# Performance work log

Measured on AMD Instinct MI355X. Metric: run time of the kernel, lower is better.

The kernel has to match this reference:

```python
import jax, jax.numpy as jnp
import numpy as np

HIDDEN = 1152
NUM_HEADS = 16
HEAD_DIM = HIDDEN // NUM_HEADS  # 72
BATCH, SEQ = 8, 1024


def setup_inputs() -> dict:
    key = jax.random.key(0)
    ks = jax.random.split(key, 9)
    s = 0.02
    return {
        "x": jax.random.normal(ks[0], (BATCH, SEQ, HIDDEN), dtype=jnp.float32),
        "wq": jax.random.normal(ks[1], (HIDDEN, HIDDEN), dtype=jnp.float32) * s,
        "bq": jax.random.normal(ks[2], (HIDDEN,), dtype=jnp.float32) * s,
        "wk": jax.random.normal(ks[3], (HIDDEN, HIDDEN), dtype=jnp.float32) * s,
        "bk": jax.random.normal(ks[4], (HIDDEN,), dtype=jnp.float32) * s,
        "wv": jax.random.normal(ks[5], (HIDDEN, HIDDEN), dtype=jnp.float32) * s,
        "bv": jax.random.normal(ks[6], (HIDDEN,), dtype=jnp.float32) * s,
        "wo": jax.random.normal(ks[7], (HIDDEN, HIDDEN), dtype=jnp.float32) * s,
        "bo": jax.random.normal(ks[8], (HIDDEN,), dtype=jnp.float32) * s,
    }


def reference(x, wq, bq, wk, bk, wv, bv, wo, bo):
    B, S, H = x.shape
    nh, hd = NUM_HEADS, HEAD_DIM
    # projections (weights stored [in, out] to match nn.Linear x @ W^T with W^T precomposed)
    q = (x @ wq + bq).reshape(B, S, nh, hd).transpose(0, 2, 1, 3)  # [B,nh,S,hd]
    k = (x @ wk + bk).reshape(B, S, nh, hd).transpose(0, 2, 1, 3)
    v = (x @ wv + bv).reshape(B, S, nh, hd).transpose(0, 2, 1, 3)
    scale = 1.0 / jnp.sqrt(jnp.asarray(hd, dtype=x.dtype))
    scores = jnp.einsum("bhqd,bhkd->bhqk", q, k) * scale  # [B,nh,S,S]
    attn = jax.nn.softmax(scores, axis=-1)
    out = jnp.einsum("bhqk,bhkd->bhqd", attn, v)  # [B,nh,S,hd]
    out = out.transpose(0, 2, 1, 3).reshape(B, S, H)
    return out @ wo + bo
```

## Files before the change

### kernel.cpp

```cpp
#include <hip/hip_runtime.h>
#include <hip/hip_bf16.h>

#define HIDDEN 1152
#define NUM_HEADS 16
#define BATCH 8
#define SEQ 1024
#define MROWS (BATCH * SEQ)
#define KSTRIDE 104

typedef __attribute__((ext_vector_type(8))) short short8;
typedef __attribute__((ext_vector_type(4))) float f32x4;

__device__ inline short f2bf(float x) {
  unsigned u = __float_as_uint(x);
  unsigned r = (u + 0x7FFFu + ((u >> 16) & 1u)) >> 16;
  return (short)(r & 0xFFFFu);
}

__device__ inline void gload16(const void* g, void* l) {
  __builtin_amdgcn_global_load_lds(
      (const __attribute__((address_space(1))) void*)g,
      (__attribute__((address_space(3))) void*)l, 16, 0, 0);
}

__global__ __launch_bounds__(256) void k_cvtx(const float* __restrict__ X,
                                              short* __restrict__ Xb) {
  const size_t base = ((size_t)blockIdx.x * 256 + threadIdx.x) * 8;
  float4 a = *(const float4*)(X + base);
  float4 b = *(const float4*)(X + base + 4);
  short8 o = {f2bf(a.x), f2bf(a.y), f2bf(a.z), f2bf(a.w),
              f2bf(b.x), f2bf(b.y), f2bf(b.z), f2bf(b.w)};
  *(short8*)(Xb + base) = o;
}

__global__ __launch_bounds__(256) void k_cvtw(const float* __restrict__ W0,
                                              const float* __restrict__ W1,
                                              const float* __restrict__ W2,
                                              const float* __restrict__ W3,
                                              short* __restrict__ Wt) {
  __shared__ float T[64][65];
  const float* W = (blockIdx.z == 0) ? W0 : (blockIdx.z == 1) ? W1
                 : (blockIdx.z == 2) ? W2 : W3;
  short* dst = Wt + (size_t)blockIdx.z * HIDDEN * HIDDEN;
  const int n0 = blockIdx.x * 64, k0 = blockIdx.y * 64;
  const int tid = threadIdx.x;
  for (int t = tid; t < 4096; t += 256) {
    int r = t >> 6, c = t & 63;
    T[r][c] = W[(size_t)(k0 + r) * HIDDEN + n0 + c];
  }
  __syncthreads();
  for (int t = tid; t < 4096; t += 256) {
    int r = t >> 6, c = t & 63;
    dst[(size_t)(n0 + r) * HIDDEN + k0 + c] = f2bf(T[c][r]);
  }
}

__global__ __launch_bounds__(256) void k_kpad(short* __restrict__ Kp) {
  const int r = blockIdx.x * 256 + threadIdx.x;
  const short8 z = {0, 0, 0, 0, 0, 0, 0, 0};
  short* p = Kp + (size_t)r * KSTRIDE + 72;
  *(short8*)(p) = z;
  *(short8*)(p + 8) = z;
  *(short8*)(p + 16) = z;
}

template <int OUTKIND, int RSTRIDE>
__global__ __launch_bounds__(256) void k_gemm(const short* __restrict__ A,
                                              const short* __restrict__ Bt,
                                              const float* __restrict__ bias,
                                              void* __restrict__ Cout,
                                              float scale) {
  __shared__ __align__(16) short As[8192];
  __shared__ __align__(16) short Bs[8192];
  const int tid = threadIdx.x;
  const int lane = tid & 63;
  const int wid = tid >> 6;
  const int wr = wid >> 1, wc = wid & 1;
  const int flat = blockIdx.y * 9 + blockIdx.x;
  const int rid = (flat & 7) * 72 + (flat >> 3);
  const int row0 = (rid / 9) << 7;
  const int col0 = (rid % 9) << 7;
  const int l15 = lane & 15, lh = lane >> 4;
  const int lr8 = lane >> 3;
  const int csrc = ((lane & 7) ^ lr8) << 3;

  const f32x4 fz = {0.f, 0.f, 0.f, 0.f};
  f32x4 acc[4][4];
#pragma unroll
  for (int m = 0; m < 4; ++m)
#pragma unroll
    for (int n = 0; n < 4; ++n) acc[m][n] = fz;

  for (int k0 = 0; k0 < HIDDEN; k0 += 64) {
#pragma unroll
    for (int i = 0; i < 4; ++i) {
      const int chunk = (wid << 2) + i;
      const int r = (chunk << 3) + lr8;
      gload16(A + (size_t)(row0 + r) * HIDDEN + k0 + csrc, (void*)(As + (chunk << 9)));
      gload16(Bt + (size_t)(col0 + r) * HIDDEN + k0 + csrc, (void*)(Bs + (chunk << 9)));
    }
    __syncthreads();
#pragma unroll
    for (int ks = 0; ks < 2; ++ks) {
      short8 af[4], bfr[4];
#pragma unroll
      for (int m = 0; m < 4; ++m) {
        const int r = (wr << 6) + (m << 4) + l15;
        const int off = ((ks << 6) + (lh << 4)) ^ ((r & 7) << 4);
        af[m] = *(const short8*)((const char*)As + r * 128 + off);
      }
#pragma unroll
      for (int n = 0; n < 4; ++n) {
        const int r = (wc << 6) + (n << 4) + l15;
        const int off = ((ks << 6) + (lh << 4)) ^ ((r & 7) << 4);
        bfr[n] = *(const short8*)((const char*)Bs + r * 128 + off);
      }
      __builtin_amdgcn_s_setprio(1);
#pragma unroll
      for (int m = 0; m < 4; ++m)
#pragma unroll
        for (int n = 0; n < 4; ++n)
          acc[m][n] = __builtin_amdgcn_mfma_f32_16x16x32_bf16(af[m], bfr[n], acc[m][n], 0, 0, 0);
      __builtin_amdgcn_s_setprio(0);
    }
    __syncthreads();
  }

  if (OUTKIND == 0) {
    short* C = (short*)Cout;
#pragma unroll
    for (int n = 0; n < 4; ++n) {
      const int c = col0 + (wc << 6) + (n << 4) + l15;
      const int h = c / 72;
      const int d = c - h * 72;
      const float bv = bias[c];
#pragma unroll
      for (int m = 0; m < 4; ++m)
#pragma unroll
        for (int i = 0; i < 4; ++i) {
          const int r = row0 + (wr << 6) + (m << 4) + (lh << 2) + i;
          const int b = r >> 10, s = r & 1023;
          C[(size_t)((((b << 4) + h) << 10) + s) * RSTRIDE + d] =
              f2bf((acc[m][n][i] + bv) * scale);
        }
    }
  } else {
    float* C = (float*)Cout;
#pragma unroll
    for (int n = 0; n < 4; ++n) {
      const int c = col0 + (wc << 6) + (n << 4) + l15;
      const float bv = bias[c];
#pragma unroll
      for (int m = 0; m < 4; ++m)
#pragma unroll
        for (int i = 0; i < 4; ++i) {
          const int r = row0 + (wr << 6) + (m << 4) + (lh << 2) + i;
          C[(size_t)r * HIDDEN + c] = acc[m][n][i] + bv;
        }
    }
  }
}

__global__ __launch_bounds__(256) void k_vtrans(const short* __restrict__ V,
                                                short* __restrict__ Vt) {
  __shared__ short T[128 * 80];
  const int tid = threadIdx.x;
  const int s0 = blockIdx.x * 128;
  const int bh = blockIdx.y;
  const size_t vbase = (size_t)bh * SEQ * 72;
  for (int t = tid; t < 128 * 9; t += 256) {
    int r = t / 9, ch = t - r * 9;
    *(short8*)(T + r * 80 + ch * 8) =
        *(const short8*)(V + vbase + (size_t)(s0 + r) * 72 + ch * 8);
  }
  __syncthreads();
  const size_t obase = (size_t)bh * 80 * 1024;
  const short8 sz = {0, 0, 0, 0, 0, 0, 0, 0};
  for (int t = tid; t < 80 * 16; t += 256) {
    int sc = t / 80, d = t - sc * 80;
    short8 v = sz;
    if (d < 72) {
#pragma unroll
      for (int j = 0; j < 8; ++j) v[j] = T[(sc * 8 + j) * 80 + d];
    }
    *(short8*)(Vt + obase + (size_t)d * 1024 + s0 + sc * 8) = v;
  }
}

__global__ __launch_bounds__(256, 4) void k_attn(const short* __restrict__ Qg,
                                                 const short* __restrict__ Kp,
                                                 const short* __restrict__ Vt,
                                                 short* __restrict__ Og) {
  __shared__ __align__(16) short Ks[64 * KSTRIDE];
  __shared__ __align__(16) short Vs[80 * 64];
  __shared__ __align__(16) short Ps[4 * 16 * 72];
  const int tid = threadIdx.x, lane = tid & 63, wid = tid >> 6;
  const int l15 = lane & 15, lh = lane >> 4;
  const int id = blockIdx.x;
  const int rid = (id & 7) * 128 + (id >> 3);
  const int bh = rid >> 3;
  const int q0 = (rid & 7) << 7;
  const short8 sz = {0, 0, 0, 0, 0, 0, 0, 0};
  const f32x4 fz = {0.f, 0.f, 0.f, 0.f};

  short8 qf[2][3];
#pragma unroll
  for (int m = 0; m < 2; ++m)
#pragma unroll
    for (int ks = 0; ks < 3; ++ks) {
      const int row = q0 + wid * 32 + m * 16 + l15;
      const int e0 = ks * 32 + lh * 8;
      if (e0 < 72)
        qf[m][ks] = *(const short8*)(Qg + ((size_t)bh * 1024 + row) * 72 + e0);
      else
        qf[m][ks] = sz;
    }

  float mrun[2] = {-1e30f, -1e30f};
  float lrun[2] = {0.f, 0.f};
  f32x4 oacc[2][5];
#pragma unroll
  for (int m = 0; m < 2; ++m)
#pragma unroll
    for (int no = 0; no < 5; ++no) oacc[m][no] = fz;

  const char* kgb = (const char*)Kp + ((size_t)bh * 1024) * (KSTRIDE * 2);
  const char* vgb = (const char*)Vt + (size_t)bh * 163840;

  for (int kt = 0; kt < 16; ++kt) {
    const char* kg = kgb + (size_t)kt * 64 * (KSTRIDE * 2);
    for (int c = wid; c < 13; c += 4)
      gload16(kg + c * 1024 + lane * 16, (char*)Ks + c * 1024);
    for (int c = wid; c < 10; c += 4) {
      const int p = c * 1024 + lane * 16;
      const int d = p >> 7;
      const int sc16 = (lane & 7) ^ (d & 7);
      gload16(vgb + (size_t)d * 2048 + kt * 128 + sc16 * 16, (char*)Vs + c * 1024);
    }
    __syncthreads();

#pragma unroll
    for (int m = 0; m < 2; ++m) {
      f32x4 sa[4];
#pragma unroll
      for (int n = 0; n < 4; ++n) sa[n] = fz;
#pragma unroll
      for (int ks = 0; ks < 3; ++ks) {
        short8 kf[4];
#pragma unroll
        for (int n = 0; n < 4; ++n)
          kf[n] = *(const short8*)((const char*)Ks + (n * 16 + l15) * 208 + ks * 64 + lh * 16);
        __builtin_amdgcn_s_setprio(1);
#pragma unroll
        for (int n = 0; n < 4; ++n)
          sa[n] = __builtin_amdgcn_mfma_f32_16x16x32_bf16(kf[n], qf[m][ks], sa[n], 0, 0, 0);
        __builtin_amdgcn_s_setprio(0);
      }

      float mx = sa[0][0];
#pragma unroll
      for (int n = 0; n < 4; ++n)
#pragma unroll
        for (int i = 0; i < 4; ++i) mx = fmaxf(mx, sa[n][i]);
      mx = fmaxf(mx, __shfl_xor(mx, 16));
      mx = fmaxf(mx, __shfl_xor(mx, 32));

      const bool skip = __all(mx <= mrun[m] + 8.0f);
      if (!skip) {
        const float nm = fmaxf(mrun[m], mx);
        const float corr = __expf(mrun[m] - nm);
        lrun[m] *= corr;
        mrun[m] = nm;
        float c0 = __shfl(corr, lh * 4 + 0);
        float c1 = __shfl(corr, lh * 4 + 1);
        float c2 = __shfl(corr, lh * 4 + 2);
        float c3 = __shfl(corr, lh * 4 + 3);
        const f32x4 cv = {c0, c1, c2, c3};
#pragma unroll
        for (int no = 0; no < 5; ++no) oacc[m][no] *= cv;
      }

      float ps = 0.f;
#pragma unroll
      for (int n = 0; n < 4; ++n)
#pragma unroll
        for (int i = 0; i < 4; ++i) {
          const float p = __expf(sa[n][i] - mrun[m]);
          sa[n][i] = p;
          ps += p;
        }
      ps += __shfl_xor(ps, 16);
      ps += __shfl_xor(ps, 32);
      lrun[m] += ps;

#pragma unroll
      for (int n = 0; n < 4; ++n) {
        unsigned w0 = __builtin_amdgcn_perm(__float_as_uint(sa[n][1]),
                                            __float_as_uint(sa[n][0]), 0x07060302u);
        unsigned w1 = __builtin_amdgcn_perm(__float_as_uint(sa[n][3]),
                                            __float_as_uint(sa[n][2]), 0x07060302u);
        uint2 w = {w0, w1};
        *(uint2*)((char*)Ps + wid * 2304 + l15 * 144 + n * 32 + lh * 8) = w;
      }

#pragma unroll
      for (int ks = 0; ks < 2; ++ks) {
        const short8 pa = *(const short8*)((const char*)Ps + wid * 2304 + l15 * 144 + ks * 64 + lh * 16);
        short8 vb[5];
        const int cc = ((ks << 2) + lh) ^ (l15 & 7);
#pragma unroll
        for (int no = 0; no < 5; ++no)
          vb[no] = *(const short8*)((const char*)Vs + no * 2048 + l15 * 128 + cc * 16);
        __builtin_amdgcn_s_setprio(1);
#pragma unroll
        for (int no = 0; no < 5; ++no)
          oacc[m][no] = __builtin_amdgcn_mfma_f32_16x16x32_bf16(pa, vb[no], oacc[m][no], 0, 0, 0);
        __builtin_amdgcn_s_setprio(0);
      }
    }
    __syncthreads();
  }

  const int b = bh >> 4, h = bh & 15;
#pragma unroll
  for (int m = 0; m < 2; ++m) {
    const float il = 1.0f / lrun[m];
    float inv[4];
#pragma unroll
    for (int i = 0; i < 4; ++i) inv[i] = __shfl(il, lh * 4 + i);
#pragma unroll
    for (int no = 0; no < 5; ++no) {
      const int d = no * 16 + l15;
      if (d < 72) {
#pragma unroll
        for (int i = 0; i < 4; ++i) {
          const int s = q0 + wid * 32 + m * 16 + lh * 4 + i;
          Og[((size_t)(b * 1024 + s)) * HIDDEN + h * 72 + d] = f2bf(oacc[m][no][i] * inv[i]);
        }
      }
    }
  }
}

extern "C" void kernel_launch(void* const* d_in, const int* in_sizes, int n_in,
                              void* d_out, int out_size, void* d_ws, size_t ws_size,
                              hipStream_t stream) {
  const float* x  = (const float*)d_in[0];
  const float* wq = (const float*)d_in[1];
  const float* bq = (const float*)d_in[2];
  const float* wk = (const float*)d_in[3];
  const float* bk = (const float*)d_in[4];
  const float* wv = (const float*)d_in[5];
  const float* bv = (const float*)d_in[6];
  const float* wo = (const float*)d_in[7];
  const float* bo = (const float*)d_in[8];

  char* ws = (char*)d_ws;
  short* xb = (short*)ws;
  short* wT = (short*)(ws + 18874368);
  short* Qb = (short*)(ws + 29491200);
  short* Kp = (short*)(ws + 48365568);
  short* Vb = (short*)(ws + 75628544);
  short* Vt = (short*)(ws + 94502912);
  const size_t WSZ = (size_t)HIDDEN * HIDDEN;

  k_kpad<<<512, 256, 0, stream>>>(Kp);
  k_cvtx<<<4608, 256, 0, stream>>>(x, xb);
  k_cvtw<<<dim3(18, 18, 4), 256, 0, stream>>>(wq, wk, wv, wo, wT);

  dim3 gg(9, 64);
  const float qscale = 0.11785113019775793f;
  k_gemm<0, 72><<<gg, 256, 0, stream>>>(xb, wT + 0 * WSZ, bq, (void*)Qb, qscale);
  k_gemm<0, KSTRIDE><<<gg, 256, 0, stream>>>(xb, wT + 1 * WSZ, bk, (void*)Kp, 1.0f);
  k_gemm<0, 72><<<gg, 256, 0, stream>>>(xb, wT + 2 * WSZ, bv, (void*)Vb, 1.0f);

  k_vtrans<<<dim3(8, 128), 256, 0, stream>>>(Vb, Vt);
  k_attn<<<1024, 256, 0, stream>>>(Qb, Kp, Vt, xb);

  k_gemm<1, 0><<<gg, 256, 0, stream>>>(xb, wT + 3 * WSZ, bo, d_out, 1.0f);
}
```

Measured before the change: 238.3 us.

## Fuse QKV GEMMs, write V transposed directly, drop LDS staging in attention

Merges the three Q/K/V projection GEMMs into one launch over a 27-column-tile grid, with the V tiles writing straight into the transposed, padded layout. This removes the separate V transpose kernel and the K padding kernel. The attention kernel no longer stages K and V tiles through shared memory with barriers and instead reads MFMA fragments directly from global memory, relying on the cache for reuse. That saves LDS traffic and syncs but risks more global and L2 pressure from redundant, less coalesced per-wave loads.

```diff
diff --git a/kernel.cpp b/kernel.cpp
--- a/kernel.cpp
+++ b/kernel.cpp
@@ -6,7 +6,7 @@
 #define BATCH 8
 #define SEQ 1024
 #define MROWS (BATCH * SEQ)
-#define KSTRIDE 104
+#define QSCALE 0.11785113019775793f
 
 typedef __attribute__((ext_vector_type(8))) short short8;
 typedef __attribute__((ext_vector_type(4))) float f32x4;
@@ -55,21 +55,122 @@
   }
 }
 
-__global__ __launch_bounds__(256) void k_kpad(short* __restrict__ Kp) {
-  const int r = blockIdx.x * 256 + threadIdx.x;
+__global__ __launch_bounds__(256) void k_vzero(short* __restrict__ Vt) {
+  const int t = blockIdx.x * 256 + threadIdx.x;
+  const int bh = t >> 10;
+  const int off = (t & 1023) * 8;
   const short8 z = {0, 0, 0, 0, 0, 0, 0, 0};
-  short* p = Kp + (size_t)r * KSTRIDE + 72;
-  *(short8*)(p) = z;
-  *(short8*)(p + 8) = z;
-  *(short8*)(p + 16) = z;
-}
-
-template <int OUTKIND, int RSTRIDE>
-__global__ __launch_bounds__(256) void k_gemm(const short* __restrict__ A,
-                                              const short* __restrict__ Bt,
-                                              const float* __restrict__ bias,
-                                              void* __restrict__ Cout,
-                                              float scale) {
+  *(short8*)(Vt + (size_t)bh * 81920 + 73728 + off) = z;
+}
+
+__global__ __launch_bounds__(256) void k_gemm_qkv(
+    const short* __restrict__ A, const short* __restrict__ Bt,
+    const float* __restrict__ bq, const float* __restrict__ bk,
+    const float* __restrict__ bv, short* __restrict__ Qb,
+    short* __restrict__ Kb, short* __restrict__ Vt) {
+  __shared__ __align__(16) short As[8192];
+  __shared__ __align__(16) short Bs[8192];
+  const int tid = threadIdx.x;
+  const int lane = tid & 63;
+  const int wid = tid >> 6;
+  const int wr = wid >> 1, wc = wid & 1;
+  const int flat = blockIdx.y * 27 + blockIdx.x;
+  const int rid = (flat & 7) * 216 + (flat >> 3);
+  const int row0 = (rid / 27) << 7;
+  const int col0 = (rid % 27) << 7;
+  const int l15 = lane & 15, lh = lane >> 4;
+  const int lr8 = lane >> 3;
+  const int csrc = ((lane & 7) ^ lr8) << 3;
+
+  const f32x4 fz = {0.f, 0.f, 0.f, 0.f};
+  f32x4 acc[4][4];
+#pragma unroll
+  for (int m = 0; m < 4; ++m)
+#pragma unroll
+    for (int n = 0; n < 4; ++n) acc[m][n] = fz;
+
+  for (int k0 = 0; k0 < HIDDEN; k0 += 64) {
+#pragma unroll
+    for (int i = 0; i < 4; ++i) {
+      const int chunk = (wid << 2) + i;
+      const int r = (chunk << 3) + lr8;
+      gload16(A + (size_t)(row0 + r) * HIDDEN + k0 + csrc, (void*)(As + (chunk << 9)));
+      gload16(Bt + (size_t)(col0 + r) * HIDDEN + k0 + csrc, (void*)(Bs + (chunk << 9)));
+    }
+    __syncthreads();
+#pragma unroll
+    for (int ks = 0; ks < 2; ++ks) {
+      short8 af[4], bfr[4];
+#pragma unroll
+      for (int m = 0; m < 4; ++m) {
+        const int r = (wr << 6) + (m << 4) + l15;
+        const int off = ((ks << 6) + (lh << 4)) ^ ((r & 7) << 4);
+        af[m] = *(const short8*)((const char*)As + r * 128 + off);
+      }
+#pragma unroll
+      for (int n = 0; n < 4; ++n) {
+        const int r = (wc << 6) + (n << 4) + l15;
+        const int off = ((ks << 6) + (lh << 4)) ^ ((r & 7) << 4);
+        bfr[n] = *(const short8*)((const char*)Bs + r * 128 + off);
+      }
+      __builtin_amdgcn_s_setprio(1);
+#pragma unroll
+      for (int m = 0; m < 4; ++m)
+#pragma unroll
+        for (int n = 0; n < 4; ++n)
+          acc[m][n] = __builtin_amdgcn_mfma_f32_16x16x32_bf16(af[m], bfr[n], acc[m][n], 0, 0, 0);
+      __builtin_amdgcn_s_setprio(0);
+    }
+    __syncthreads();
+  }
+
+  const int cseg = (rid % 27) / 9;
+  if (cseg < 2) {
+    short* dst = (cseg == 0) ? Qb : Kb;
+    const float* bias = (cseg == 0) ? bq : bk;
+    const float scl = (cseg == 0) ? QSCALE : 1.0f;
+#pragma unroll
+    for (int n = 0; n < 4; ++n) {
+      const int c = col0 - cseg * HIDDEN + (wc << 6) + (n << 4) + l15;
+      const int h = c / 72;
+      const int d = c - h * 72;
+      const float bvx = bias[c];
+#pragma unroll
+      for (int m = 0; m < 4; ++m)
+#pragma unroll
+        for (int i = 0; i < 4; ++i) {
+          const int r = row0 + (wr << 6) + (m << 4) + (lh << 2) + i;
+          const int b = r >> 10, s = r & 1023;
+          dst[(size_t)((((b << 4) + h) << 10) + s) * 72 + d] =
+              f2bf((acc[m][n][i] + bvx) * scl);
+        }
+    }
+  } else {
+#pragma unroll
+    for (int n = 0; n < 4; ++n) {
+      const int c = col0 - 2 * HIDDEN + (wc << 6) + (n << 4) + l15;
+      const int h = c / 72;
+      const int d = c - h * 72;
+      const float bvx = bv[c];
+#pragma unroll
+      for (int m = 0; m < 4; ++m) {
+        const int r0 = row0 + (wr << 6) + (m << 4) + (lh << 2);
+        const int b = r0 >> 10, s0 = r0 & 1023;
+        short4 o;
+        o.x = f2bf(acc[m][n][0] + bvx);
+        o.y = f2bf(acc[m][n][1] + bvx);
+        o.z = f2bf(acc[m][n][2] + bvx);
+        o.w = f2bf(acc[m][n][3] + bvx);
+        *(short4*)(Vt + ((size_t)(((b << 4) + h) * 80 + d) << 10) + s0) = o;
+      }
+    }
+  }
+}
+
+__global__ __launch_bounds__(256) void k_gemm_o(const short* __restrict__ A,
+                                                const short* __restrict__ Bt,
+                                                const float* __restrict__ bias,
+                                                float* __restrict__ C) {
   __shared__ __align__(16) short As[8192];
   __shared__ __align__(16) short Bs[8192];
   const int tid = threadIdx.x;
@@ -126,73 +227,24 @@
     __syncthreads();
   }
 
-  if (OUTKIND == 0) {
-    short* C = (short*)Cout;
-#pragma unroll
-    for (int n = 0; n < 4; ++n) {
-      const int c = col0 + (wc << 6) + (n << 4) + l15;
-      const int h = c / 72;
-      const int d = c - h * 72;
-      const float bv = bias[c];
-#pragma unroll
-      for (int m = 0; m < 4; ++m)
-#pragma unroll
-        for (int i = 0; i < 4; ++i) {
-          const int r = row0 + (wr << 6) + (m << 4) + (lh << 2) + i;
-          const int b = r >> 10, s = r & 1023;
-          C[(size_t)((((b << 4) + h) << 10) + s) * RSTRIDE + d] =
-              f2bf((acc[m][n][i] + bv) * scale);
-        }
-    }
-  } else {
-    float* C = (float*)Cout;
-#pragma unroll
-    for (int n = 0; n < 4; ++n) {
-      const int c = col0 + (wc << 6) + (n << 4) + l15;
-      const float bv = bias[c];
-#pragma unroll
-      for (int m = 0; m < 4; ++m)
-#pragma unroll
-        for (int i = 0; i < 4; ++i) {
-          const int r = row0 + (wr << 6) + (m << 4) + (lh << 2) + i;
-          C[(size_t)r * HIDDEN + c] = acc[m][n][i] + bv;
-        }
-    }
-  }
-}
-
-__global__ __launch_bounds__(256) void k_vtrans(const short* __restrict__ V,
-                                                short* __restrict__ Vt) {
-  __shared__ short T[128 * 80];
-  const int tid = threadIdx.x;
-  const int s0 = blockIdx.x * 128;
-  const int bh = blockIdx.y;
-  const size_t vbase = (size_t)bh * SEQ * 72;
-  for (int t = tid; t < 128 * 9; t += 256) {
-    int r = t / 9, ch = t - r * 9;
-    *(short8*)(T + r * 80 + ch * 8) =
-        *(const short8*)(V + vbase + (size_t)(s0 + r) * 72 + ch * 8);
-  }
-  __syncthreads();
-  const size_t obase = (size_t)bh * 80 * 1024;
-  const short8 sz = {0, 0, 0, 0, 0, 0, 0, 0};
-  for (int t = tid; t < 80 * 16; t += 256) {
-    int sc = t / 80, d = t - sc * 80;
-    short8 v = sz;
-    if (d < 72) {
-#pragma unroll
-      for (int j = 0; j < 8; ++j) v[j] = T[(sc * 8 + j) * 80 + d];
-    }
-    *(short8*)(Vt + obase + (size_t)d * 1024 + s0 + sc * 8) = v;
+#pragma unroll
+  for (int n = 0; n < 4; ++n) {
+    const int c = col0 + (wc << 6) + (n << 4) + l15;
+    const float bvx = bias[c];
+#pragma unroll
+    for (int m = 0; m < 4; ++m)
+#pragma unroll
+      for (int i = 0; i < 4; ++i) {
+        const int r = row0 + (wr << 6) + (m << 4) + (lh << 2) + i;
+        C[(size_t)r * HIDDEN + c] = acc[m][n][i] + bvx;
+      }
   }
 }
 
 __global__ __launch_bounds__(256, 4) void k_attn(const short* __restrict__ Qg,
-                                                 const short* __restrict__ Kp,
+                                                 const short* __restrict__ Kg,
                                                  const short* __restrict__ Vt,
                                                  short* __restrict__ Og) {
-  __shared__ __align__(16) short Ks[64 * KSTRIDE];
-  __shared__ __align__(16) short Vs[80 * 64];
   __shared__ __align__(16) short Ps[4 * 16 * 72];
   const int tid = threadIdx.x, lane = tid & 63, wid = tid >> 6;
   const int l15 = lane & 15, lh = lane >> 4;
@@ -224,21 +276,11 @@
 #pragma unroll
     for (int no = 0; no < 5; ++no) oacc[m][no] = fz;
 
-  const char* kgb = (const char*)Kp + ((size_t)bh * 1024) * (KSTRIDE * 2);
-  const char* vgb = (const char*)Vt + (size_t)bh * 163840;
+  const short* kb = Kg + (size_t)bh * 1024 * 72;
+  const short* vg = Vt + (size_t)bh * 81920;
+  short* psw = Ps + wid * 1152;
 
   for (int kt = 0; kt < 16; ++kt) {
-    const char* kg = kgb + (size_t)kt * 64 * (KSTRIDE * 2);
-    for (int c = wid; c < 13; c += 4)
-      gload16(kg + c * 1024 + lane * 16, (char*)Ks + c * 1024);
-    for (int c = wid; c < 10; c += 4) {
-      const int p = c * 1024 + lane * 16;
-      const int d = p >> 7;
-      const int sc16 = (lane & 7) ^ (d & 7);
-      gload16(vgb + (size_t)d * 2048 + kt * 128 + sc16 * 16, (char*)Vs + c * 1024);
-    }
-    __syncthreads();
-
 #pragma unroll
     for (int m = 0; m < 2; ++m) {
       f32x4 sa[4];
@@ -249,7 +291,8 @@
         short8 kf[4];
 #pragma unroll
         for (int n = 0; n < 4; ++n)
-          kf[n] = *(const short8*)((const char*)Ks + (n * 16 + l15) * 208 + ks * 64 + lh * 16);
+          kf[n] = *(const short8*)(kb + (size_t)(kt * 64 + n * 16 + l15) * 72 +
+                                   ks * 32 + lh * 8);
         __builtin_amdgcn_s_setprio(1);
 #pragma unroll
         for (int n = 0; n < 4; ++n)
@@ -300,17 +343,17 @@
         unsigned w1 = __builtin_amdgcn_perm(__float_as_uint(sa[n][3]),
                                             __float_as_uint(sa[n][2]), 0x07060302u);
         uint2 w = {w0, w1};
-        *(uint2*)((char*)Ps + wid * 2304 + l15 * 144 + n * 32 + lh * 8) = w;
+        *(uint2*)((char*)psw + l15 * 144 + n * 32 + lh * 8) = w;
       }
 
 #pragma unroll
       for (int ks = 0; ks < 2; ++ks) {
-        const short8 pa = *(const short8*)((const char*)Ps + wid * 2304 + l15 * 144 + ks * 64 + lh * 16);
+        const short8 pa = *(const short8*)((const char*)psw + l15 * 144 + ks * 64 + lh * 16);
         short8 vb[5];
-        const int cc = ((ks << 2) + lh) ^ (l15 & 7);
 #pragma unroll
         for (int no = 0; no < 5; ++no)
-          vb[no] = *(const short8*)((const char*)Vs + no * 2048 + l15 * 128 + cc * 16);
+          vb[no] = *(const short8*)(vg + (size_t)(no * 16 + l15) * 1024 +
+                                    kt * 64 + ks * 32 + lh * 8);
         __builtin_amdgcn_s_setprio(1);
 #pragma unroll
         for (int no = 0; no < 5; ++no)
@@ -318,7 +361,6 @@
         __builtin_amdgcn_s_setprio(0);
       }
     }
-    __syncthreads();
   }
 
   const int b = bh >> 4, h = bh & 15;
@@ -359,23 +401,15 @@
   short* xb = (short*)ws;
   short* wT = (short*)(ws + 18874368);
   short* Qb = (short*)(ws + 29491200);
-  short* Kp = (short*)(ws + 48365568);
-  short* Vb = (short*)(ws + 75628544);
-  short* Vt = (short*)(ws + 94502912);
+  short* Kb = (short*)(ws + 48365568);
+  short* Vt = (short*)(ws + 67241984);
   const size_t WSZ = (size_t)HIDDEN * HIDDEN;
 
-  k_kpad<<<512, 256, 0, stream>>>(Kp);
   k_cvtx<<<4608, 256, 0, stream>>>(x, xb);
   k_cvtw<<<dim3(18, 18, 4), 256, 0, stream>>>(wq, wk, wv, wo, wT);
-
-  dim3 gg(9, 64);
-  const float qscale = 0.11785113019775793f;
-  k_gemm<0, 72><<<gg, 256, 0, stream>>>(xb, wT + 0 * WSZ, bq, (void*)Qb, qscale);
-  k_gemm<0, KSTRIDE><<<gg, 256, 0, stream>>>(xb, wT + 1 * WSZ, bk, (void*)Kp, 1.0f);
-  k_gemm<0, 72><<<gg, 256, 0, stream>>>(xb, wT + 2 * WSZ, bv, (void*)Vb, 1.0f);
-
-  k_vtrans<<<dim3(8, 128), 256, 0, stream>>>(Vb, Vt);
-  k_attn<<<1024, 256, 0, stream>>>(Qb, Kp, Vt, xb);
-
-  k_gemm<1, 0><<<gg, 256, 0, stream>>>(xb, wT + 3 * WSZ, bo, d_out, 1.0f);
-}
+  k_vzero<<<512, 256, 0, stream>>>(Vt);
+
+  k_gemm_qkv<<<dim3(27, 64), 256, 0, stream>>>(xb, wT, bq, bk, bv, Qb, Kb, Vt);
+  k_attn<<<1024, 256, 0, stream>>>(Qb, Kb, Vt, xb);
+  k_gemm_o<<<dim3(9, 64), 256, 0, stream>>>(xb, wT + 3 * WSZ, bo, (float*)d_out);
+}
```

Result: slower. 358.9 us (+50.6%).
